# Kernel tuning notes

Measured on AMD Instinct MI355X. Metric: run time of the kernel, lower is better.

## Reference

```python
import jax, jax.numpy as jnp
import numpy as np

MASK_VALUE = -10000000.0

def reference(query, key, value, valid_length):
    # query: (B,n,d), key: (B,m,d), value: (B,m,dv), valid_length: (B,)
    d = key.shape[2]
    scale = 1.0 / jnp.sqrt(jnp.asarray(d, dtype=query.dtype))
    scores = jnp.einsum('bnd,bmd->bnm', query, key) * scale  # (B,n,m)
    m = key.shape[1]
    # mask positions >= valid_length per batch element
    mask = jnp.arange(m)[None, None, :] >= valid_length[:, None, None]  # (B,1,m)
    scores = jnp.where(mask, MASK_VALUE, scores)
    attn = jax.nn.softmax(scores, axis=-1)
    return jnp.einsum('bnm,bmv->bnv', attn, value)

def setup_inputs() -> dict:
    key = jax.random.key(0)
    k1, k2, k3, k4 = jax.random.split(key, 4)
    B, n, m, d, dv = 16, 1024, 1024, 128, 128
    return {
        'query': jax.random.normal(k1, (B, n, d), dtype=jnp.float32),
        'key': jax.random.normal(k2, (B, m, d), dtype=jnp.float32),
        'value': jax.random.normal(k3, (B, m, dv), dtype=jnp.float32),
        'valid_length': jax.random.randint(k4, (B,), 1, m + 1, dtype=jnp.int32),
    }
```

## Files before the change

### kernel.cpp

```cpp
#include <hip/hip_runtime.h>
#include <hip/hip_bf16.h>

typedef __attribute__((ext_vector_type(4))) float f32x4;
typedef __attribute__((ext_vector_type(8))) short s16x8;
typedef unsigned int u32;

#define DHEAD 128
#define KVB 32
#define BLKQ 64
#define NGRP 4
#define TILB 8192
#define LDSZ 133120

__device__ __forceinline__ short f2bf(float x) {
    __hip_bfloat16 h = __float2bfloat16(x);
    return *reinterpret_cast<short*>(&h);
}

__global__ __launch_bounds__(256)
void prep_frag(const float* __restrict__ K, const float* __restrict__ V,
               const int* __restrict__ VL,
               short* __restrict__ Kz, short* __restrict__ Vz, int m, int NT, int nkf) {
    const int i = blockIdx.x * 256 + threadIdx.x;
    if (i < nkf) {
        const int lane = i & 63;
        const int kk   = (i >> 6) & 3;
        const int s    = (i >> 8) & 1;
        const int rest = i >> 9;
        const int t = rest % NT, b = rest / NT;
        if (t * KVB >= VL[b]) return;
        const int qi = lane & 15, g = lane >> 4;
        const float* src = K + (size_t)(b * m + t * KVB + 16 * s + qi) * DHEAD + kk * 32 + g * 8;
        f32x4 a = *reinterpret_cast<const f32x4*>(src);
        f32x4 c = *reinterpret_cast<const f32x4*>(src + 4);
        s16x8 o;
        #pragma unroll
        for (int j = 0; j < 4; ++j) { o[j] = f2bf(a[j]); o[4 + j] = f2bf(c[j]); }
        *reinterpret_cast<s16x8*>(Kz + (size_t)i * 8) = o;
    } else {
        const int j = i - nkf;
        if (j < nkf) {
            const int lane = j & 63;
            const int dg   = (j >> 6) & 7;
            const int rest = j >> 9;
            const int t = rest % NT, b = rest / NT;
            if (t * KVB >= VL[b]) return;
            const int qi = lane & 15, g = lane >> 4;
            const float* vb = V + (size_t)(b * m + t * KVB + g * 4) * DHEAD + dg * 16 + qi;
            s16x8 o;
            #pragma unroll
            for (int r = 0; r < 4; ++r) {
                o[r]     = f2bf(vb[(size_t)r * DHEAD]);
                o[4 + r] = f2bf(vb[(size_t)(16 + r) * DHEAD]);
            }
            *reinterpret_cast<s16x8*>(Vz + (size_t)j * 8) = o;
        }
    }
}

__global__ __launch_bounds__(1024, 4)
void attn_fwd(const float* __restrict__ Q, const short* __restrict__ Kz,
              const short* __restrict__ Vz, const int* __restrict__ VL,
              float* __restrict__ O, int B, int n, int NT) {
    extern __shared__ char lds[];

    const int tid   = threadIdx.x;
    const int lane  = tid & 63;
    const int wid   = tid >> 6;
    const int qslot = wid & 3;
    const int grp   = wid >> 2;
    const int gl    = lane >> 4;
    const int qi    = lane & 15;

    const int nq = n / BLKQ;
    int b, qt;
    if ((B & 7) == 0) {
        const int xcd = blockIdx.x & 7;
        const int sub = blockIdx.x >> 3;
        const int bpx = B >> 3;
        b  = xcd * bpx + (sub % bpx);
        qt = sub / bpx;
    } else {
        b = blockIdx.x / nq; qt = blockIdx.x % nq;
    }

    const int vl = VL[b];
    const int nt = (vl + KVB - 1) / KVB;
    const int IT = (nt + NGRP - 1) / NGRP;
    const int rowbase = b * n + qt * BLKQ + qslot * 16;

    const float qsc = 0.08838834764831845f * 1.4426950408889634f;
    s16x8 qf[4];
    {
        const float* qp = Q + (size_t)(rowbase + qi) * DHEAD + gl * 8;
        #pragma unroll
        for (int kk = 0; kk < 4; ++kk) {
            f32x4 a  = *reinterpret_cast<const f32x4*>(qp + kk * 32);
            f32x4 cc = *reinterpret_cast<const f32x4*>(qp + kk * 32 + 4);
            s16x8 s;
            #pragma unroll
            for (int j = 0; j < 4; ++j) { s[j] = f2bf(a[j] * qsc); s[4 + j] = f2bf(cc[j] * qsc); }
            qf[kk] = s;
        }
    }

    const char* KzB = (const char*)Kz + (size_t)b * NT * TILB;
    const char* VzB = (const char*)Vz + (size_t)b * NT * TILB;

    auto DMA = [&](int buf, int t) {
        const char* ks = KzB + (size_t)t * TILB;
        const char* vs = VzB + (size_t)t * TILB;
        char* dst = &lds[grp * 32768 + buf * 16384];
        const int off = qslot * 2048;
        #pragma unroll
        for (int j = 0; j < 2; ++j) {
            __builtin_amdgcn_global_load_lds(
                (const __attribute__((address_space(1))) u32*)(ks + off + j * 1024 + lane * 16),
                (__attribute__((address_space(3))) u32*)(dst + off + j * 1024), 16, 0, 0);
            __builtin_amdgcn_global_load_lds(
                (const __attribute__((address_space(1))) u32*)(vs + off + j * 1024 + lane * 16),
                (__attribute__((address_space(3))) u32*)(dst + 8192 + off + j * 1024), 16, 0, 0);
        }
    };

    f32x4 Oacc[8];
    #pragma unroll
    for (int dg = 0; dg < 8; ++dg) Oacc[dg] = 0.f;
    float llocal = 0.f;
    const int lb = lane * 16;

    if (grp < nt) DMA(0, grp);
    __syncthreads();

    int cur = 0;
    #pragma unroll 1
    for (int i = 0; i < IT; ++i) {
        const int t  = grp + i * NGRP;
        const int tn = t + NGRP;
        if (tn < nt) DMA(cur ^ 1, tn);

        if (t < nt) {
            const char* ksb = &lds[grp * 32768 + cur * 16384];
            const char* vsb = ksb + 8192;

            f32x4 Sacc[2];
            Sacc[0] = 0.f; Sacc[1] = 0.f;
            __builtin_amdgcn_s_setprio(1);
            #pragma unroll
            for (int s = 0; s < 2; ++s)
                #pragma unroll
                for (int kk = 0; kk < 4; ++kk) {
                    s16x8 kf = *reinterpret_cast<const s16x8*>(ksb + (s * 4 + kk) * 1024 + lb);
                    Sacc[s] = __builtin_amdgcn_mfma_f32_16x16x32_bf16(kf, qf[kk], Sacc[s], 0, 0, 0);
                }
            __builtin_amdgcn_s_setprio(0);

            const int kvrem = vl - t * KVB;
            if (kvrem < KVB) {
                #pragma unroll
                for (int s = 0; s < 2; ++s)
                    #pragma unroll
                    for (int r = 0; r < 4; ++r)
                        if (s * 16 + gl * 4 + r >= kvrem) Sacc[s][r] = -1e30f;
            }

            s16x8 pa;
            #pragma unroll
            for (int s = 0; s < 2; ++s)
                #pragma unroll
                for (int r = 0; r < 4; ++r) {
                    const float e = __builtin_amdgcn_exp2f(fminf(Sacc[s][r], 60.f));
                    llocal += e;
                    pa[s * 4 + r] = f2bf(e);
                }

            __builtin_amdgcn_s_setprio(1);
            #pragma unroll
            for (int dg = 0; dg < 8; ++dg) {
                s16x8 vf = *reinterpret_cast<const s16x8*>(vsb + dg * 1024 + lb);
                Oacc[dg] = __builtin_amdgcn_mfma_f32_16x16x32_bf16(pa, vf, Oacc[dg], 0, 0, 0);
            }
            __builtin_amdgcn_s_setprio(0);
        }

        __syncthreads();
        cur ^= 1;
    }

    llocal += __shfl_xor(llocal, 16);
    llocal += __shfl_xor(llocal, 32);

    float* P    = (float*)lds;
    float* lred = (float*)&lds[131072];
    {
        float* w = P + (((size_t)(grp * 4 + qslot)) * 8) * 256;
        #pragma unroll
        for (int dg = 0; dg < 8; ++dg)
            *reinterpret_cast<f32x4*>(w + dg * 256 + lane * 4) = Oacc[dg];
        if (gl == 0) lred[grp * 64 + qslot * 16 + qi] = llocal;
    }
    __syncthreads();

    {
        float ltot = 0.f;
        #pragma unroll
        for (int g2 = 0; g2 < 4; ++g2) ltot += lred[g2 * 64 + qslot * 16 + qi];
        const float linv = 1.0f / ltot;
        const float l0 = __shfl(linv, gl * 4 + 0);
        const float l1 = __shfl(linv, gl * 4 + 1);
        const float l2 = __shfl(linv, gl * 4 + 2);
        const float l3 = __shfl(linv, gl * 4 + 3);

        float* Ob = O + (size_t)rowbase * DHEAD;
        #pragma unroll
        for (int k = 0; k < 2; ++k) {
            const int dg = grp * 2 + k;
            f32x4 acc = 0.f;
            #pragma unroll
            for (int g2 = 0; g2 < 4; ++g2) {
                const float* rp = P + (((size_t)(g2 * 4 + qslot)) * 8 + dg) * 256 + lane * 4;
                f32x4 v = *reinterpret_cast<const f32x4*>(rp);
                acc[0] += v[0]; acc[1] += v[1]; acc[2] += v[2]; acc[3] += v[3];
            }
            Ob[(gl * 4 + 0) * DHEAD + dg * 16 + qi] = acc[0] * l0;
            Ob[(gl * 4 + 1) * DHEAD + dg * 16 + qi] = acc[1] * l1;
            Ob[(gl * 4 + 2) * DHEAD + dg * 16 + qi] = acc[2] * l2;
            Ob[(gl * 4 + 3) * DHEAD + dg * 16 + qi] = acc[3] * l3;
        }
    }
}

extern "C" void kernel_launch(void* const* d_in, const int* in_sizes, int n_in,
                              void* d_out, int out_size, void* d_ws, size_t ws_size,
                              hipStream_t stream) {
    const float* Q  = (const float*)d_in[0];
    const float* K  = (const float*)d_in[1];
    const float* V  = (const float*)d_in[2];
    const int*   VL = (const int*)d_in[3];
    float* O = (float*)d_out;

    const int B = in_sizes[3];
    const int n = in_sizes[0] / (B * DHEAD);
    const int m = in_sizes[1] / (B * DHEAD);
    const int NT = m / KVB;

    short* Kz = (short*)d_ws;
    short* Vz = Kz + (size_t)B * NT * (TILB / 2);

    const int nkf = B * NT * 512;
    prep_frag<<<(2 * nkf + 255) / 256, 256, 0, stream>>>(K, V, VL, Kz, Vz, m, NT, nkf);

    hipFuncSetAttribute((const void*)attn_fwd,
                        hipFuncAttributeMaxDynamicSharedMemorySize, LDSZ);
    const int grid = B * (n / BLKQ);
    attn_fwd<<<grid, 1024, LDSZ, stream>>>(Q, Kz, Vz, VL, O, B, n, NT);
}
```

Measured before the change: 26.73 us.

## Halve waves per block; each wave computes two 16-row query slices

The block shrinks from 16 waves to 8, and each wave now holds two 16-row query tiles. Each K and V fragment read from LDS therefore feeds two MFMAs. The DMA loop is widened so fewer waves still load the whole tile, and the final reduction covers both virtual query slots per wave. The aim is to halve LDS fragment reads per MFMA, at the cost of more registers per wave (two sets of O accumulators) and fewer waves to hide latency.

```diff
diff --git a/kernel.cpp b/kernel.cpp
--- a/kernel.cpp
+++ b/kernel.cpp
@@ -58,7 +58,7 @@
     }
 }
 
-__global__ __launch_bounds__(1024, 4)
+__global__ __launch_bounds__(512, 2)
 void attn_fwd(const float* __restrict__ Q, const short* __restrict__ Kz,
               const short* __restrict__ Vz, const int* __restrict__ VL,
               float* __restrict__ O, int B, int n, int NT) {
@@ -67,8 +67,8 @@
     const int tid   = threadIdx.x;
     const int lane  = tid & 63;
     const int wid   = tid >> 6;
-    const int qslot = wid & 3;
-    const int grp   = wid >> 2;
+    const int qslot = wid & 1;
+    const int grp   = wid >> 1;
     const int gl    = lane >> 4;
     const int qi    = lane & 15;
 
@@ -87,20 +87,26 @@
     const int vl = VL[b];
     const int nt = (vl + KVB - 1) / KVB;
     const int IT = (nt + NGRP - 1) / NGRP;
-    const int rowbase = b * n + qt * BLKQ + qslot * 16;
+    const int rowbase = b * n + qt * BLKQ + qslot * 32;
 
     const float qsc = 0.08838834764831845f * 1.4426950408889634f;
-    s16x8 qf[4];
+    s16x8 qf0[4], qf1[4];
     {
-        const float* qp = Q + (size_t)(rowbase + qi) * DHEAD + gl * 8;
+        const float* qp0 = Q + (size_t)(rowbase + qi) * DHEAD + gl * 8;
+        const float* qp1 = qp0 + 16 * DHEAD;
         #pragma unroll
         for (int kk = 0; kk < 4; ++kk) {
-            f32x4 a  = *reinterpret_cast<const f32x4*>(qp + kk * 32);
-            f32x4 cc = *reinterpret_cast<const f32x4*>(qp + kk * 32 + 4);
-            s16x8 s;
-            #pragma unroll
-            for (int j = 0; j < 4; ++j) { s[j] = f2bf(a[j] * qsc); s[4 + j] = f2bf(cc[j] * qsc); }
-            qf[kk] = s;
+            f32x4 a0 = *reinterpret_cast<const f32x4*>(qp0 + kk * 32);
+            f32x4 c0 = *reinterpret_cast<const f32x4*>(qp0 + kk * 32 + 4);
+            f32x4 a1 = *reinterpret_cast<const f32x4*>(qp1 + kk * 32);
+            f32x4 c1 = *reinterpret_cast<const f32x4*>(qp1 + kk * 32 + 4);
+            s16x8 s0, s1;
+            #pragma unroll
+            for (int j = 0; j < 4; ++j) {
+                s0[j] = f2bf(a0[j] * qsc); s0[4 + j] = f2bf(c0[j] * qsc);
+                s1[j] = f2bf(a1[j] * qsc); s1[4 + j] = f2bf(c1[j] * qsc);
+            }
+            qf0[kk] = s0; qf1[kk] = s1;
         }
     }
 
@@ -111,9 +117,9 @@
         const char* ks = KzB + (size_t)t * TILB;
         const char* vs = VzB + (size_t)t * TILB;
         char* dst = &lds[grp * 32768 + buf * 16384];
-        const int off = qslot * 2048;
-        #pragma unroll
-        for (int j = 0; j < 2; ++j) {
+        const int off = qslot * 4096;
+        #pragma unroll
+        for (int j = 0; j < 4; ++j) {
             __builtin_amdgcn_global_load_lds(
                 (const __attribute__((address_space(1))) u32*)(ks + off + j * 1024 + lane * 16),
                 (__attribute__((address_space(3))) u32*)(dst + off + j * 1024), 16, 0, 0);
@@ -123,10 +129,10 @@
         }
     };
 
-    f32x4 Oacc[8];
+    f32x4 Oacc0[8], Oacc1[8];
     #pragma unroll
-    for (int dg = 0; dg < 8; ++dg) Oacc[dg] = 0.f;
-    float llocal = 0.f;
+    for (int dg = 0; dg < 8; ++dg) { Oacc0[dg] = 0.f; Oacc1[dg] = 0.f; }
+    float ll0 = 0.f, ll1 = 0.f;
     const int lb = lane * 16;
 
     if (grp < nt) DMA(0, grp);
@@ -143,15 +149,16 @@
             const char* ksb = &lds[grp * 32768 + cur * 16384];
             const char* vsb = ksb + 8192;
 
-            f32x4 Sacc[2];
-            Sacc[0] = 0.f; Sacc[1] = 0.f;
+            f32x4 Sa0[2], Sa1[2];
+            Sa0[0] = 0.f; Sa0[1] = 0.f; Sa1[0] = 0.f; Sa1[1] = 0.f;
             __builtin_amdgcn_s_setprio(1);
             #pragma unroll
             for (int s = 0; s < 2; ++s)
                 #pragma unroll
                 for (int kk = 0; kk < 4; ++kk) {
                     s16x8 kf = *reinterpret_cast<const s16x8*>(ksb + (s * 4 + kk) * 1024 + lb);
-                    Sacc[s] = __builtin_amdgcn_mfma_f32_16x16x32_bf16(kf, qf[kk], Sacc[s], 0, 0, 0);
+                    Sa0[s] = __builtin_amdgcn_mfma_f32_16x16x32_bf16(kf, qf0[kk], Sa0[s], 0, 0, 0);
+                    Sa1[s] = __builtin_amdgcn_mfma_f32_16x16x32_bf16(kf, qf1[kk], Sa1[s], 0, 0, 0);
                 }
             __builtin_amdgcn_s_setprio(0);
 
@@ -161,24 +168,27 @@
                 for (int s = 0; s < 2; ++s)
                     #pragma unroll
                     for (int r = 0; r < 4; ++r)
-                        if (s * 16 + gl * 4 + r >= kvrem) Sacc[s][r] = -1e30f;
-            }
-
-            s16x8 pa;
+                        if (s * 16 + gl * 4 + r >= kvrem) { Sa0[s][r] = -1e30f; Sa1[s][r] = -1e30f; }
+            }
+
+            s16x8 pa0, pa1;
             #pragma unroll
             for (int s = 0; s < 2; ++s)
                 #pragma unroll
                 for (int r = 0; r < 4; ++r) {
-                    const float e = __builtin_amdgcn_exp2f(fminf(Sacc[s][r], 60.f));
-                    llocal += e;
-                    pa[s * 4 + r] = f2bf(e);
+                    const float e0 = __builtin_amdgcn_exp2f(fminf(Sa0[s][r], 60.f));
+                    const float e1 = __builtin_amdgcn_exp2f(fminf(Sa1[s][r], 60.f));
+                    ll0 += e0; ll1 += e1;
+                    pa0[s * 4 + r] = f2bf(e0);
+                    pa1[s * 4 + r] = f2bf(e1);
                 }
 
             __builtin_amdgcn_s_setprio(1);
             #pragma unroll
             for (int dg = 0; dg < 8; ++dg) {
                 s16x8 vf = *reinterpret_cast<const s16x8*>(vsb + dg * 1024 + lb);
-                Oacc[dg] = __builtin_amdgcn_mfma_f32_16x16x32_bf16(pa, vf, Oacc[dg], 0, 0, 0);
+                Oacc0[dg] = __builtin_amdgcn_mfma_f32_16x16x32_bf16(pa0, vf, Oacc0[dg], 0, 0, 0);
+                Oacc1[dg] = __builtin_amdgcn_mfma_f32_16x16x32_bf16(pa1, vf, Oacc1[dg], 0, 0, 0);
             }
             __builtin_amdgcn_s_setprio(0);
         }
@@ -187,38 +197,47 @@
         cur ^= 1;
     }
 
-    llocal += __shfl_xor(llocal, 16);
-    llocal += __shfl_xor(llocal, 32);
+    ll0 += __shfl_xor(ll0, 16); ll0 += __shfl_xor(ll0, 32);
+    ll1 += __shfl_xor(ll1, 16); ll1 += __shfl_xor(ll1, 32);
 
     float* P    = (float*)lds;
     float* lred = (float*)&lds[131072];
+    const int vq0 = qslot * 2, vq1 = vq0 + 1;
     {
-        float* w = P + (((size_t)(grp * 4 + qslot)) * 8) * 256;
-        #pragma unroll
-        for (int dg = 0; dg < 8; ++dg)
-            *reinterpret_cast<f32x4*>(w + dg * 256 + lane * 4) = Oacc[dg];
-        if (gl == 0) lred[grp * 64 + qslot * 16 + qi] = llocal;
+        float* w0 = P + (((size_t)(grp * 4 + vq0)) * 8) * 256;
+        float* w1 = P + (((size_t)(grp * 4 + vq1)) * 8) * 256;
+        #pragma unroll
+        for (int dg = 0; dg < 8; ++dg) {
+            *reinterpret_cast<f32x4*>(w0 + dg * 256 + lane * 4) = Oacc0[dg];
+            *reinterpret_cast<f32x4*>(w1 + dg * 256 + lane * 4) = Oacc1[dg];
+        }
+        if (gl == 0) {
+            lred[grp * 64 + vq0 * 16 + qi] = ll0;
+            lred[grp * 64 + vq1 * 16 + qi] = ll1;
+        }
     }
     __syncthreads();
 
-    {
+    #pragma unroll
+    for (int h = 0; h < 2; ++h) {
+        const int vq = qslot * 2 + h;
         float ltot = 0.f;
         #pragma unroll
-        for (int g2 = 0; g2 < 4; ++g2) ltot += lred[g2 * 64 + qslot * 16 + qi];
+        for (int g2 = 0; g2 < 4; ++g2) ltot += lred[g2 * 64 + vq * 16 + qi];
         const float linv = 1.0f / ltot;
         const float l0 = __shfl(linv, gl * 4 + 0);
         const float l1 = __shfl(linv, gl * 4 + 1);
         const float l2 = __shfl(linv, gl * 4 + 2);
         const float l3 = __shfl(linv, gl * 4 + 3);
 
-        float* Ob = O + (size_t)rowbase * DHEAD;
+        float* Ob = O + (size_t)(b * n + qt * BLKQ + vq * 16) * DHEAD;
         #pragma unroll
         for (int k = 0; k < 2; ++k) {
             const int dg = grp * 2 + k;
             f32x4 acc = 0.f;
             #pragma unroll
             for (int g2 = 0; g2 < 4; ++g2) {
-                const float* rp = P + (((size_t)(g2 * 4 + qslot)) * 8 + dg) * 256 + lane * 4;
+                const float* rp = P + (((size_t)(g2 * 4 + vq)) * 8 + dg) * 256 + lane * 4;
                 f32x4 v = *reinterpret_cast<const f32x4*>(rp);
                 acc[0] += v[0]; acc[1] += v[1]; acc[2] += v[2]; acc[3] += v[3];
             }
@@ -253,5 +272,5 @@
     hipFuncSetAttribute((const void*)attn_fwd,
                         hipFuncAttributeMaxDynamicSharedMemorySize, LDSZ);
     const int grid = B * (n / BLKQ);
-    attn_fwd<<<grid, 1024, LDSZ, stream>>>(Q, Kz, Vz, VL, O, B, n, NT);
-}
+    attn_fwd<<<grid, 512, LDSZ, stream>>>(Q, Kz, Vz, VL, O, B, n, NT);
+}
```

Result: no change. 27.17 us (+1.7%).

## Halve KV and query tiles, use 512-thread blocks with zero-padded PV MFMA

Applied to the files above, without the earlier changes.

Shrinks the KV tile from 32 to 16 keys and the query block from 64 to 32 rows. Blocks drop to 512 threads with halved LDS use, so more blocks can be resident per CU and the grid doubles. V fragments are repacked as 4-element halves, and the PV MFMA runs with half of its K dimension zero-padded. This wastes half of that MFMA's throughput and doubles K/V reloads per query row, in exchange for finer masking granularity and better occupancy and load balance.

```diff
diff --git a/kernel.cpp b/kernel.cpp
--- a/kernel.cpp
+++ b/kernel.cpp
@@ -3,14 +3,16 @@
 
 typedef __attribute__((ext_vector_type(4))) float f32x4;
 typedef __attribute__((ext_vector_type(8))) short s16x8;
+typedef __attribute__((ext_vector_type(4))) short s16x4;
 typedef unsigned int u32;
 
 #define DHEAD 128
-#define KVB 32
-#define BLKQ 64
+#define KVB 16
+#define BLKQ 32
 #define NGRP 4
-#define TILB 8192
-#define LDSZ 133120
+#define KTB 4096
+#define VTB 4096
+#define LDSZ 66048
 
 __device__ __forceinline__ short f2bf(float x) {
     __hip_bfloat16 h = __float2bfloat16(x);
@@ -20,17 +22,18 @@
 __global__ __launch_bounds__(256)
 void prep_frag(const float* __restrict__ K, const float* __restrict__ V,
                const int* __restrict__ VL,
-               short* __restrict__ Kz, short* __restrict__ Vz, int m, int NT, int nkf) {
+               short* __restrict__ Kz, short* __restrict__ Vz,
+               int m, int NT32, int NT16, int nkf, int nvf) {
     const int i = blockIdx.x * 256 + threadIdx.x;
     if (i < nkf) {
         const int lane = i & 63;
         const int kk   = (i >> 6) & 3;
         const int s    = (i >> 8) & 1;
         const int rest = i >> 9;
-        const int t = rest % NT, b = rest / NT;
-        if (t * KVB >= VL[b]) return;
+        const int t = rest % NT32, b = rest / NT32;
+        if (t * 32 >= VL[b]) return;
         const int qi = lane & 15, g = lane >> 4;
-        const float* src = K + (size_t)(b * m + t * KVB + 16 * s + qi) * DHEAD + kk * 32 + g * 8;
+        const float* src = K + (size_t)(b * m + t * 32 + 16 * s + qi) * DHEAD + kk * 32 + g * 8;
         f32x4 a = *reinterpret_cast<const f32x4*>(src);
         f32x4 c = *reinterpret_cast<const f32x4*>(src + 4);
         s16x8 o;
@@ -39,36 +42,33 @@
         *reinterpret_cast<s16x8*>(Kz + (size_t)i * 8) = o;
     } else {
         const int j = i - nkf;
-        if (j < nkf) {
+        if (j < nvf) {
             const int lane = j & 63;
             const int dg   = (j >> 6) & 7;
             const int rest = j >> 9;
-            const int t = rest % NT, b = rest / NT;
-            if (t * KVB >= VL[b]) return;
+            const int tau = rest % NT16, b = rest / NT16;
+            if (tau * KVB >= VL[b]) return;
             const int qi = lane & 15, g = lane >> 4;
-            const float* vb = V + (size_t)(b * m + t * KVB + g * 4) * DHEAD + dg * 16 + qi;
-            s16x8 o;
-            #pragma unroll
-            for (int r = 0; r < 4; ++r) {
-                o[r]     = f2bf(vb[(size_t)r * DHEAD]);
-                o[4 + r] = f2bf(vb[(size_t)(16 + r) * DHEAD]);
-            }
-            *reinterpret_cast<s16x8*>(Vz + (size_t)j * 8) = o;
-        }
-    }
-}
-
-__global__ __launch_bounds__(1024, 4)
+            const float* vb = V + (size_t)(b * m + tau * KVB + g * 4) * DHEAD + dg * 16 + qi;
+            s16x4 o;
+            #pragma unroll
+            for (int r = 0; r < 4; ++r) o[r] = f2bf(vb[(size_t)r * DHEAD]);
+            *reinterpret_cast<s16x4*>(Vz + (size_t)j * 4) = o;
+        }
+    }
+}
+
+__global__ __launch_bounds__(512, 2)
 void attn_fwd(const float* __restrict__ Q, const short* __restrict__ Kz,
               const short* __restrict__ Vz, const int* __restrict__ VL,
-              float* __restrict__ O, int B, int n, int NT) {
+              float* __restrict__ O, int B, int n, int NT16) {
     extern __shared__ char lds[];
 
     const int tid   = threadIdx.x;
     const int lane  = tid & 63;
     const int wid   = tid >> 6;
-    const int qslot = wid & 3;
-    const int grp   = wid >> 2;
+    const int qslot = wid & 1;
+    const int grp   = wid >> 1;
     const int gl    = lane >> 4;
     const int qi    = lane & 15;
 
@@ -85,7 +85,7 @@
     }
 
     const int vl = VL[b];
-    const int nt = (vl + KVB - 1) / KVB;
+    const int nt = (vl + KVB - 1) >> 4;
     const int IT = (nt + NGRP - 1) / NGRP;
     const int rowbase = b * n + qt * BLKQ + qslot * 16;
 
@@ -104,22 +104,17 @@
         }
     }
 
-    const char* KzB = (const char*)Kz + (size_t)b * NT * TILB;
-    const char* VzB = (const char*)Vz + (size_t)b * NT * TILB;
-
-    auto DMA = [&](int buf, int t) {
-        const char* ks = KzB + (size_t)t * TILB;
-        const char* vs = VzB + (size_t)t * TILB;
-        char* dst = &lds[grp * 32768 + buf * 16384];
-        const int off = qslot * 2048;
-        #pragma unroll
-        for (int j = 0; j < 2; ++j) {
+    const char* KzB = (const char*)Kz + (size_t)b * NT16 * KTB;
+    const char* VzB = (const char*)Vz + (size_t)b * NT16 * VTB;
+
+    auto DMA = [&](int buf, int tau) {
+        const char* src = (qslot ? VzB : KzB) + (size_t)tau * 4096;
+        char* dst = &lds[grp * 16384 + buf * 8192 + qslot * 4096];
+        #pragma unroll
+        for (int j = 0; j < 4; ++j) {
             __builtin_amdgcn_global_load_lds(
-                (const __attribute__((address_space(1))) u32*)(ks + off + j * 1024 + lane * 16),
-                (__attribute__((address_space(3))) u32*)(dst + off + j * 1024), 16, 0, 0);
-            __builtin_amdgcn_global_load_lds(
-                (const __attribute__((address_space(1))) u32*)(vs + off + j * 1024 + lane * 16),
-                (__attribute__((address_space(3))) u32*)(dst + 8192 + off + j * 1024), 16, 0, 0);
+                (const __attribute__((address_space(1))) u32*)(src + j * 1024 + lane * 16),
+                (__attribute__((address_space(3))) u32*)(dst + j * 1024), 16, 0, 0);
         }
     };
 
@@ -135,49 +130,46 @@
     int cur = 0;
     #pragma unroll 1
     for (int i = 0; i < IT; ++i) {
-        const int t  = grp + i * NGRP;
-        const int tn = t + NGRP;
+        const int tau = grp + i * NGRP;
+        const int tn  = tau + NGRP;
         if (tn < nt) DMA(cur ^ 1, tn);
 
-        if (t < nt) {
-            const char* ksb = &lds[grp * 32768 + cur * 16384];
-            const char* vsb = ksb + 8192;
-
-            f32x4 Sacc[2];
-            Sacc[0] = 0.f; Sacc[1] = 0.f;
+        if (tau < nt) {
+            const char* ksb = &lds[grp * 16384 + cur * 8192];
+            const char* vsb = ksb + 4096;
+
+            f32x4 Sacc = 0.f;
             __builtin_amdgcn_s_setprio(1);
             #pragma unroll
-            for (int s = 0; s < 2; ++s)
-                #pragma unroll
-                for (int kk = 0; kk < 4; ++kk) {
-                    s16x8 kf = *reinterpret_cast<const s16x8*>(ksb + (s * 4 + kk) * 1024 + lb);
-                    Sacc[s] = __builtin_amdgcn_mfma_f32_16x16x32_bf16(kf, qf[kk], Sacc[s], 0, 0, 0);
-                }
+            for (int kk = 0; kk < 4; ++kk) {
+                s16x8 kf = *reinterpret_cast<const s16x8*>(ksb + kk * 1024 + lb);
+                Sacc = __builtin_amdgcn_mfma_f32_16x16x32_bf16(kf, qf[kk], Sacc, 0, 0, 0);
+            }
             __builtin_amdgcn_s_setprio(0);
 
-            const int kvrem = vl - t * KVB;
+            const int kvrem = vl - tau * KVB;
             if (kvrem < KVB) {
                 #pragma unroll
-                for (int s = 0; s < 2; ++s)
-                    #pragma unroll
-                    for (int r = 0; r < 4; ++r)
-                        if (s * 16 + gl * 4 + r >= kvrem) Sacc[s][r] = -1e30f;
+                for (int r = 0; r < 4; ++r)
+                    if (gl * 4 + r >= kvrem) Sacc[r] = -1e30f;
             }
 
             s16x8 pa;
             #pragma unroll
-            for (int s = 0; s < 2; ++s)
-                #pragma unroll
-                for (int r = 0; r < 4; ++r) {
-                    const float e = __builtin_amdgcn_exp2f(fminf(Sacc[s][r], 60.f));
-                    llocal += e;
-                    pa[s * 4 + r] = f2bf(e);
-                }
+            for (int r = 0; r < 4; ++r) {
+                const float e = __builtin_amdgcn_exp2f(fminf(Sacc[r], 60.f));
+                llocal += e;
+                pa[r]     = f2bf(e);
+                pa[4 + r] = 0;
+            }
 
             __builtin_amdgcn_s_setprio(1);
             #pragma unroll
             for (int dg = 0; dg < 8; ++dg) {
-                s16x8 vf = *reinterpret_cast<const s16x8*>(vsb + dg * 1024 + lb);
+                s16x4 v4 = *reinterpret_cast<const s16x4*>(vsb + dg * 512 + lane * 8);
+                s16x8 vf;
+                vf[0] = v4[0]; vf[1] = v4[1]; vf[2] = v4[2]; vf[3] = v4[3];
+                vf[4] = 0; vf[5] = 0; vf[6] = 0; vf[7] = 0;
                 Oacc[dg] = __builtin_amdgcn_mfma_f32_16x16x32_bf16(pa, vf, Oacc[dg], 0, 0, 0);
             }
             __builtin_amdgcn_s_setprio(0);
@@ -191,20 +183,21 @@
     llocal += __shfl_xor(llocal, 32);
 
     float* P    = (float*)lds;
-    float* lred = (float*)&lds[131072];
+    float* lred = (float*)&lds[65536];
+    const int s8 = grp * 2 + qslot;
     {
-        float* w = P + (((size_t)(grp * 4 + qslot)) * 8) * 256;
+        float* w = P + ((size_t)s8 * 8) * 256;
         #pragma unroll
         for (int dg = 0; dg < 8; ++dg)
             *reinterpret_cast<f32x4*>(w + dg * 256 + lane * 4) = Oacc[dg];
-        if (gl == 0) lred[grp * 64 + qslot * 16 + qi] = llocal;
+        if (gl == 0) lred[s8 * 16 + qi] = llocal;
     }
     __syncthreads();
 
     {
         float ltot = 0.f;
         #pragma unroll
-        for (int g2 = 0; g2 < 4; ++g2) ltot += lred[g2 * 64 + qslot * 16 + qi];
+        for (int g2 = 0; g2 < 4; ++g2) ltot += lred[(g2 * 2 + qslot) * 16 + qi];
         const float linv = 1.0f / ltot;
         const float l0 = __shfl(linv, gl * 4 + 0);
         const float l1 = __shfl(linv, gl * 4 + 1);
@@ -218,7 +211,7 @@
             f32x4 acc = 0.f;
             #pragma unroll
             for (int g2 = 0; g2 < 4; ++g2) {
-                const float* rp = P + (((size_t)(g2 * 4 + qslot)) * 8 + dg) * 256 + lane * 4;
+                const float* rp = P + ((size_t)(g2 * 2 + qslot) * 8 + dg) * 256 + lane * 4;
                 f32x4 v = *reinterpret_cast<const f32x4*>(rp);
                 acc[0] += v[0]; acc[1] += v[1]; acc[2] += v[2]; acc[3] += v[3];
             }
@@ -242,16 +235,19 @@
     const int B = in_sizes[3];
     const int n = in_sizes[0] / (B * DHEAD);
     const int m = in_sizes[1] / (B * DHEAD);
-    const int NT = m / KVB;
+    const int NT32 = m / 32;
+    const int NT16 = m / KVB;
 
     short* Kz = (short*)d_ws;
-    short* Vz = Kz + (size_t)B * NT * (TILB / 2);
-
-    const int nkf = B * NT * 512;
-    prep_frag<<<(2 * nkf + 255) / 256, 256, 0, stream>>>(K, V, VL, Kz, Vz, m, NT, nkf);
+    short* Vz = Kz + (size_t)B * NT16 * (KTB / 2);
+
+    const int nkf = B * NT32 * 512;
+    const int nvf = B * NT16 * 512;
+    prep_frag<<<(nkf + nvf + 255) / 256, 256, 0, stream>>>(K, V, VL, Kz, Vz,
+                                                           m, NT32, NT16, nkf, nvf);
 
     hipFuncSetAttribute((const void*)attn_fwd,
                         hipFuncAttributeMaxDynamicSharedMemorySize, LDSZ);
     const int grid = B * (n / BLKQ);
-    attn_fwd<<<grid, 1024, LDSZ, stream>>>(Q, Kz, Vz, VL, O, B, n, NT);
-}
+    attn_fwd<<<grid, 512, LDSZ, stream>>>(Q, Kz, Vz, VL, O, B, n, NT16);
+}
```

After: 29.02 us. 1.09x slower.
